# Kernel tuning notes

Hardware: AMD Instinct MI355X
Metric: run time of the kernel (lower is better)

Reference implementation:

```python
import jax, jax.numpy as jnp
import numpy as np

B, L = 16, 2048          # batch, raw history length
H, S, M = 512, 8, 512    # hidden_dim, sequence_count, max_seq_len
V = 32000                # shared embed_tokens vocab
TG = 64                  # TIME_GAP_BUCKET_COUNT
LN_EPS = 1e-5


def setup_inputs() -> dict:
    key = jax.random.key(0)
    ks = jax.random.split(key, 16)
    f = lambda k, shp, scale=0.02: jax.random.normal(k, shp, jnp.float32) * scale
    return {
        "history_tokens": jax.random.randint(ks[0], (B, L), 0, V),
        "history_post_tokens": jax.random.randint(ks[1], (B, L), 0, V),
        "history_author_tokens": jax.random.randint(ks[2], (B, L), 0, V),
        "history_action_tokens": jax.random.randint(ks[3], (B, L), 0, V),
        "history_time_gap": jax.random.randint(ks[4], (B, L), 0, TG + 1),
        "history_group_ids": jax.random.randint(ks[5], (B, L), 0, S + 1),
        "history_mask": jax.random.randint(ks[6], (B, L), 0, 2).astype(bool),
        "embed_table": f(ks[7], (V, H)),
        "time_gap_table": f(ks[8], (TG + 1, H)).at[0].set(0.0),   # padding_idx=0
        "seq_id_table": f(ks[9], (S + 1, H)).at[0].set(0.0),      # padding_idx=0
        "pos_table": f(ks[10], (M, H)),
        "ln_gamma": jnp.ones((5 * H,), jnp.float32),
        "ln_beta": jnp.zeros((5 * H,), jnp.float32),
        "w1": f(ks[11], (5 * H, 4 * H)),
        "b1": jnp.zeros((4 * H,), jnp.float32),
        "w2": f(ks[12], (4 * H, H)),
        "b2": jnp.zeros((H,), jnp.float32),
        "empty_tokens": f(ks[13], (S, H)),
    }


def _forward(embed_table, time_gap_table, seq_id_table, pos_table, ln_gamma, ln_beta,
             w1, b1, w2, b2, empty_tokens,
             history_tokens, history_post_tokens, history_author_tokens,
             history_action_tokens, history_time_gap, history_group_ids, history_mask):
    # --- event feature construction: 4 shared-vocab lookups + time-gap embedding ---
    h = embed_table[history_tokens]            # [B,L,H]
    p = embed_table[history_post_tokens]
    a = embed_table[history_author_tokens]
    act = embed_table[history_action_tokens]
    gap_idx = jnp.clip(history_time_gap, 0, TG)
    gap = time_gap_table[gap_idx] * (gap_idx != 0)[..., None]  # padding_idx=0 -> zero vec
    x = jnp.concatenate([h, p, a, act, gap], axis=-1)           # [B,L,5H]

    # --- event_projection: LayerNorm -> Linear -> SiLU -> (Dropout eval) -> Linear ---
    mu = x.mean(-1, keepdims=True)
    var = x.var(-1, keepdims=True)
    xn = (x - mu) * jax.lax.rsqrt(var + LN_EPS) * ln_gamma + ln_beta
    mid = jax.nn.silu(xn @ w1 + b1)                             # [B,L,4H]
    event = mid @ w2 + b2                                       # [B,L,H]

    # --- ragged regroup: for each (b, s) gather masked positions with group id s+1,
    #     keep the LAST M of them, scatter to slots 0..count-1 ---
    gid = history_group_ids                                     # [B,L]
    match = history_mask[:, None, :] & (gid[:, None, :] == jnp.arange(1, S + 1)[None, :, None])  # [B,S,L]
    cum = jnp.cumsum(match.astype(jnp.int32), axis=-1)          # rank+1 within group
    count = cum[..., -1]                                        # [B,S]
    offset = jnp.maximum(count - M, 0)                          # drop all but last M
    slot = cum - 1 - offset[..., None]                          # [B,S,L]
    keep = match & (slot >= 0)
    slot = jnp.where(keep, slot, M)                             # M is out-of-range -> dropped

    b_idx = jnp.arange(B)[:, None, None]
    s_idx = jnp.arange(S)[None, :, None]
    states = jnp.zeros((B, S, M, H), event.dtype)
    states = states.at[b_idx, s_idx, slot].set(event[:, None, :, :], mode="drop")
    smask = jnp.zeros((B, S, M), bool)
    smask = smask.at[b_idx, s_idx, slot].set(True, mode="drop")

    # empty groups get the learned empty token at slot 0
    empty = count == 0                                          # [B,S]
    states = states.at[:, :, 0, :].set(
        jnp.where(empty[..., None], empty_tokens[None], states[:, :, 0, :]))
    smask = smask.at[:, :, 0].set(smask[:, :, 0] | empty)

    # positional + sequence-id embeddings, then zero padded slots
    pos = pos_table[None, None]                                 # [1,1,M,H]
    sid = seq_id_table[1:S + 1][None, :, None, :]               # [1,S,1,H]
    states = (states + pos + sid) * smask[..., None].astype(states.dtype)
    return states, smask


def reference(history_tokens, history_post_tokens, history_author_tokens,
              history_action_tokens, history_time_gap, history_group_ids, history_mask,
              embed_table, time_gap_table, seq_id_table, pos_table, ln_gamma, ln_beta,
              w1, b1, w2, b2, empty_tokens):
    return _forward(embed_table, time_gap_table, seq_id_table, pos_table, ln_gamma, ln_beta,
                    w1, b1, w2, b2, empty_tokens,
                    history_tokens, history_post_tokens, history_author_tokens,
                    history_action_tokens, history_time_gap, history_group_ids, history_mask)
```

## Files before the change

kernel.cpp:

```cpp
#include <hip/hip_runtime.h>
#include <hip/hip_bf16.h>
#include <stdint.h>

#define B_ 16
#define L_ 2048
#define H_ 512
#define S_ 8
#define M_ 512
#define TG_ 64
#define NTOK (B_ * L_)
#define FIVEH (5 * H_)
#define FOURH (4 * H_)

typedef __attribute__((ext_vector_type(4))) float f32x4;
typedef __attribute__((ext_vector_type(8))) short bf16x8;

__device__ __forceinline__ short f2bf(float f) {
  unsigned u = __builtin_bit_cast(unsigned, f);
  unsigned r = (u + 0x7FFFu + ((u >> 16) & 1u)) >> 16;
  return (short)r;
}

__device__ __forceinline__ void gload_lds16(const void* g, void* l) {
  __builtin_amdgcn_global_load_lds(
      (const __attribute__((address_space(1))) unsigned int*)g,
      (__attribute__((address_space(3))) unsigned int*)l, 16, 0, 0);
}

#define BAR __builtin_amdgcn_s_barrier()
#define LGKM0 do { asm volatile("s_waitcnt lgkmcnt(0)" ::: "memory"); \
                   __builtin_amdgcn_sched_barrier(0); } while (0)
#define VMW(n) asm volatile("s_waitcnt vmcnt(" #n ")" ::: "memory")
#define PRIO(p) __builtin_amdgcn_s_setprio(p)


#define STAGE(src, isB, slot, half, kt) do {                                  \
    const short* _s = (src) + (size_t)((half) * 128) * K + (kt);              \
    const int _o = ((isB) ? 65536 : 0) + (slot) * 32768 + (half) * 16384;     \
    gload_lds16(_s + (size_t)sr0 * K + sc0, lds + _o + db0);                  \
    gload_lds16(_s + (size_t)sr1 * K + sc1, lds + _o + db1);                  \
  } while (0)

#define LDA(qr, slot) do { const int _b = (slot) * 32768 + aW + (qr) * 8192;  \
    _Pragma("unroll") for (int fm = 0; fm < 4; ++fm)                          \
    _Pragma("unroll") for (int ks = 0; ks < 2; ++ks)                          \
      a[fm][ks] = *(const bf16x8*)(lds + _b + sA[fm][ks]); } while (0)

#define LDB(dst, qc, slot) do { const int _b = (slot) * 32768 + bW + (qc) * 4096; \
    _Pragma("unroll") for (int fn = 0; fn < 2; ++fn)                          \
    _Pragma("unroll") for (int ks = 0; ks < 2; ++ks)                          \
      dst[fn][ks] = *(const bf16x8*)(lds + _b + sB[fn][ks]); } while (0)

#define MFMA16(qr, qc, bs) do {                                               \
    _Pragma("unroll") for (int fm = 0; fm < 4; ++fm)                          \
    _Pragma("unroll") for (int fn = 0; fn < 2; ++fn)                          \
    _Pragma("unroll") for (int ks = 0; ks < 2; ++ks)                          \
      acc[(qr)*4+fm][(qc)*2+fn] = __builtin_amdgcn_mfma_f32_16x16x32_bf16(    \
          a[fm][ks], bs[fn][ks], acc[(qr)*4+fm][(qc)*2+fn], 0, 0, 0); } while (0)

template<int K>
__device__ __forceinline__ void gemm_core(const short* __restrict__ Ag,
                                          const short* __restrict__ Bg,
                                          char* lds, f32x4 (&acc)[8][4],
                                          int tid) {
  constexpr int NITER = K / 128;
  const int lane = tid & 63;
  const int wave = tid >> 6;
  const int wm = wave >> 2;
  const int wn = wave & 3;
  const int la = lane & 15;
  const int hi = lane >> 4;

  const int x = (la & 7) << 4;
  int sA[4][2], sB[2][2];
#pragma unroll
  for (int fm = 0; fm < 4; ++fm)
#pragma unroll
    for (int ks = 0; ks < 2; ++ks)
      sA[fm][ks] = (((fm * 16 + la) * 128) + (ks * 32 + hi * 8) * 2) ^ x;
#pragma unroll
  for (int fn = 0; fn < 2; ++fn)
#pragma unroll
    for (int ks = 0; ks < 2; ++ks)
      sB[fn][ks] = ((((wn & 1) * 64 + fn * 16 + la) * 128) + (ks * 32 + hi * 8) * 2) ^ x;
  const int aW = wm * 16384;
  const int bW = 65536 + (wn >> 1) * 16384;

  const int db0 = tid * 16, db1 = tid * 16 + 8192;
  const int lb0 = db0 ^ (((db0 >> 7) & 7) << 4);
  const int lb1 = db1 ^ (((db1 >> 7) & 7) << 4);
  const int sr0 = lb0 >> 7, sc0 = (lb0 & 127) >> 1;
  const int sr1 = lb1 >> 7, sc1 = (lb1 & 127) >> 1;

  bf16x8 a[4][2], b0v[2][2], b1v[2][2];

  STAGE(Bg, 1, 0, 0, 0); STAGE(Bg, 1, 0, 1, 0);
  STAGE(Ag, 0, 0, 0, 0); STAGE(Ag, 0, 0, 1, 0);
  STAGE(Bg, 1, 1, 0, 64); STAGE(Bg, 1, 1, 1, 64);
  VMW(0);
  BAR;

  for (int i = 0; i < NITER - 1; ++i) {
    const int kt1 = (2 * i + 1) * 64, kt2 = kt1 + 64, kt3 = kt1 + 128;
    LDA(0, 0); LDB(b0v, 0, 0); STAGE(Ag, 0, 1, 0, kt1);
    BAR; LGKM0; PRIO(1); MFMA16(0, 0, b0v); PRIO(0); BAR;
    LDB(b1v, 1, 0); STAGE(Ag, 0, 1, 1, kt1);
    BAR; LGKM0; PRIO(1); MFMA16(0, 1, b1v); PRIO(0); BAR;
    LDA(1, 0); STAGE(Bg, 1, 0, 0, kt2);
    BAR; LGKM0; PRIO(1); MFMA16(1, 1, b1v); PRIO(0); BAR;
    STAGE(Bg, 1, 0, 1, kt2);
    BAR; LGKM0; PRIO(1); MFMA16(1, 0, b0v); PRIO(0); VMW(4); BAR;
    LDA(0, 1); LDB(b0v, 0, 1); STAGE(Ag, 0, 0, 0, kt2);
    BAR; LGKM0; PRIO(1); MFMA16(0, 0, b0v); PRIO(0); BAR;
    LDB(b1v, 1, 1); STAGE(Ag, 0, 0, 1, kt2);
    BAR; LGKM0; PRIO(1); MFMA16(0, 1, b1v); PRIO(0); BAR;
    LDA(1, 1); STAGE(Bg, 1, 1, 0, kt3);
    BAR; LGKM0; PRIO(1); MFMA16(1, 1, b1v); PRIO(0); BAR;
    STAGE(Bg, 1, 1, 1, kt3);
    BAR; LGKM0; PRIO(1); MFMA16(1, 0, b0v); PRIO(0); VMW(4); BAR;
  }
  {
    const int kt1 = (2 * (NITER - 1) + 1) * 64;
    LDA(0, 0); LDB(b0v, 0, 0); STAGE(Ag, 0, 1, 0, kt1);
    BAR; LGKM0; PRIO(1); MFMA16(0, 0, b0v); PRIO(0); BAR;
    LDB(b1v, 1, 0); STAGE(Ag, 0, 1, 1, kt1);
    BAR; LGKM0; PRIO(1); MFMA16(0, 1, b1v); PRIO(0); BAR;
    LDA(1, 0);
    BAR; LGKM0; PRIO(1); MFMA16(1, 1, b1v); PRIO(0); BAR;
    BAR; LGKM0; PRIO(1); MFMA16(1, 0, b0v); PRIO(0); VMW(0); BAR;
    LDA(0, 1); LDB(b0v, 0, 1);
    BAR; LGKM0; PRIO(1); MFMA16(0, 0, b0v); PRIO(0); BAR;
    LDB(b1v, 1, 1);
    BAR; LGKM0; PRIO(1); MFMA16(0, 1, b1v); PRIO(0); BAR;
    LDA(1, 1);
    BAR; LGKM0; PRIO(1); MFMA16(1, 1, b1v); PRIO(0); BAR;
    BAR; LGKM0; PRIO(1); MFMA16(1, 0, b0v); PRIO(0);
  }
}

__global__ __launch_bounds__(512, 2) void gemm1_kernel(
    const short* __restrict__ A, const short* __restrict__ Bt,
    const float* __restrict__ bias, const int* __restrict__ nkeep,
    short* __restrict__ C) {
  const int nbm = (nkeep[0] + 255) >> 8;
  const int local = blockIdx.x >> 3;
  if (local >= nbm) return;
  const int T = (blockIdx.x & 7) * nbm + local;
  const int bm = T >> 3, bn = T & 7;
  __shared__ __align__(16) char lds[131072];
  const int tid = threadIdx.x;
  f32x4 acc[8][4] = {};
  gemm_core<FIVEH>(A + (size_t)bm * 256 * FIVEH, Bt + (size_t)bn * 256 * FIVEH,
                   lds, acc, tid);
  const int lane = tid & 63, wave = tid >> 6;
  const int wm = wave >> 2, wn = wave & 3;
  const int la = lane & 15, hi = lane >> 4;
  const int row0 = bm * 256 + wm * 128 + hi * 4;
  const int col0 = bn * 256 + wn * 64 + la;
#pragma unroll
  for (int mi = 0; mi < 8; ++mi)
#pragma unroll
    for (int ni = 0; ni < 4; ++ni) {
      const int col = col0 + ni * 16;
      const float bv = bias[col];
#pragma unroll
      for (int r = 0; r < 4; ++r) {
        const int row = row0 + mi * 16 + r;
        float v = acc[mi][ni][r] + bv;
        float sg = 1.f / (1.f + __expf(-v));
        C[(size_t)row * FOURH + col] = f2bf(v * sg);
      }
    }
}

#define ASL(s) ((s) * 32768)
#define BSL(s) (98304 + (s) * 16384)

#define STG2(src, ldsoff, kt) do {                                            \
    const short* _s = (src) + (kt);                                          \
    gload_lds16(_s + (size_t)sr0 * 2048 + sc0, lds + (ldsoff) + db0);         \
    gload_lds16(_s + (size_t)sr1 * 2048 + sc1, lds + (ldsoff) + db1);         \
  } while (0)

#define LDA2(slot) do { const int _b = ASL(slot) + aW2;                       \
    _Pragma("unroll") for (int fm = 0; fm < 4; ++fm)                          \
    _Pragma("unroll") for (int ks = 0; ks < 2; ++ks)                          \
      a[fm][ks] = *(const bf16x8*)(lds + _b + sA2[fm][ks]); } while (0)

#define LDB2a(slot) do { const int _b = BSL(slot);                            \
    _Pragma("unroll") for (int fn = 0; fn < 2; ++fn)                          \
    _Pragma("unroll") for (int ks = 0; ks < 2; ++ks)                          \
      b[fn][ks] = *(const bf16x8*)(lds + _b + sB2[fn][ks]); } while (0)

#define LDB2b(slot) do { const int _b = BSL(slot);                            \
    _Pragma("unroll") for (int fn = 2; fn < 4; ++fn)                          \
    _Pragma("unroll") for (int ks = 0; ks < 2; ++ks)                          \
      b[fn][ks] = *(const bf16x8*)(lds + _b + sB2[fn][ks]); } while (0)

#define MFMA2(h) do {                                                         \
    _Pragma("unroll") for (int fm = 0; fm < 4; ++fm)                          \
    _Pragma("unroll") for (int fn = 2*(h); fn < 2*(h)+2; ++fn)                \
    _Pragma("unroll") for (int ks = 0; ks < 2; ++ks)                          \
      acc[fm][fn] = __builtin_amdgcn_mfma_f32_16x16x32_bf16(                  \
          a[fm][ks], b[fn][ks], acc[fm][fn], 0, 0, 0); } while (0)

#define T2(slot, kt, ISSUE, WAITC) do {                                       \
    LDA2(slot); LDB2a(slot);                                                  \
    if (ISSUE) STG2(Ag, ASL(((slot) + 2) % 3), kt);                           \
    BAR; LGKM0; PRIO(1); MFMA2(0); PRIO(0); BAR;                              \
    LDB2b(slot);                                                              \
    if (ISSUE) { STG2(Ag + 128 * 2048, ASL(((slot) + 2) % 3) + 16384, kt);    \
                 STG2(Bg, BSL(((slot) + 2) % 3), kt); }                       \
    BAR; LGKM0; PRIO(1); MFMA2(1); PRIO(0); WAITC; BAR;                       \
  } while (0)

__global__ __launch_bounds__(512) void gemm2fin_kernel(
    const short* __restrict__ A, const short* __restrict__ Bt,
    const float* __restrict__ b2, const float* __restrict__ pos,
    const float* __restrict__ sidtab, const int* __restrict__ destv,
    const int* __restrict__ nkeep, const int* __restrict__ counts,
    const float* __restrict__ empty_tok, float* __restrict__ states,
    float* __restrict__ smask) {
  if (blockIdx.x >= 512) {
    const int total = B_ * S_ * M_ * (H_ / 4);
    for (int idx = (blockIdx.x - 512) * 512 + threadIdx.x; idx < total;
         idx += 512 * 512) {
      const int row = idx >> 7, c = idx & 127;
      const int gs = row >> 9, m = row & (M_ - 1), s = gs & (S_ - 1);
      const int cnt = counts[gs];
      const bool empty = (cnt == 0);
      const bool filled = m < (cnt < M_ ? cnt : M_);
      if (c == 0) smask[row] = (filled || (empty && m == 0)) ? 1.0f : 0.0f;
      if (filled) continue;
      float4 o = make_float4(0.f, 0.f, 0.f, 0.f);
      if (empty && m == 0) {
        float4 e = ((const float4*)(empty_tok + s * H_))[c];
        float4 pv = ((const float4*)pos)[c];
        float4 sd = ((const float4*)(sidtab + (s + 1) * H_))[c];
        o.x = e.x + pv.x + sd.x;
        o.y = e.y + pv.y + sd.y;
        o.z = e.z + pv.z + sd.z;
        o.w = e.w + pv.w + sd.w;
      }
      ((float4*)(states + (size_t)row * H_))[c] = o;
    }
    return;
  }
  const int nk = nkeep[0];
  const int ntile = ((nk + 255) >> 8) << 2;
  const int q = ntile >> 3, r = ntile & 7;
  const int xg = blockIdx.x & 7, idx = blockIdx.x >> 3;
  const int cntx = q + (xg < r ? 1 : 0);
  if (idx >= cntx) return;
  const int T = xg * q + (xg < r ? xg : r) + idx;
  const int bm = T >> 2, bn = T & 3;
  __shared__ __align__(16) char lds[147456];
  const int tid = threadIdx.x;
  const int lane = tid & 63, wave = tid >> 6;
  const int wm = wave >> 1;
  const int wn = wave & 1;
  const int la = lane & 15, hi = lane >> 4;
  const short* Ag = A + (size_t)bm * 256 * 2048;
  const short* Bg = Bt + (size_t)bn * 128 * 2048;

  const int x = (la & 7) << 4;
  int sA2[4][2], sB2[4][2];
#pragma unroll
  for (int fm = 0; fm < 4; ++fm)
#pragma unroll
    for (int ks = 0; ks < 2; ++ks)
      sA2[fm][ks] = ((((wm & 1) * 64 + fm * 16 + la) * 128) + (ks * 32 + hi * 8) * 2) ^ x;
#pragma unroll
  for (int fn = 0; fn < 4; ++fn)
#pragma unroll
    for (int ks = 0; ks < 2; ++ks)
      sB2[fn][ks] = (((wn * 64 + fn * 16 + la) * 128) + (ks * 32 + hi * 8) * 2) ^ x;
  const int aW2 = (wm >> 1) * 16384;

  const int db0 = tid * 16, db1 = tid * 16 + 8192;
  const int lb0 = db0 ^ (((db0 >> 7) & 7) << 4);
  const int lb1 = db1 ^ (((db1 >> 7) & 7) << 4);
  const int sr0 = lb0 >> 7, sc0 = (lb0 & 127) >> 1;
  const int sr1 = lb1 >> 7, sc1 = (lb1 & 127) >> 1;

  f32x4 acc[4][4] = {};
  bf16x8 a[4][2], b[4][2];

  STG2(Ag, ASL(0), 0); STG2(Ag + 128 * 2048, ASL(0) + 16384, 0); STG2(Bg, BSL(0), 0);
  STG2(Ag, ASL(1), 64); STG2(Ag + 128 * 2048, ASL(1) + 16384, 64); STG2(Bg, BSL(1), 64);
  VMW(6);
  BAR;
  for (int i = 0; i < 10; ++i) {
    const int kt = i * 192 + 128;
    T2(0, kt, true, VMW(6));
    T2(1, kt + 64, true, VMW(6));
    T2(2, kt + 128, true, VMW(6));
  }
  T2(0, 0, false, VMW(0));
  T2(1, 0, false, ((void)0));

  const int row0 = bm * 256 + wm * 64 + hi * 4;
  const int col0 = bn * 128 + wn * 64 + la;
#pragma unroll
  for (int mi = 0; mi < 4; ++mi) {
#pragma unroll
    for (int r2 = 0; r2 < 4; ++r2) {
      const int row = row0 + mi * 16 + r2;
      if (row >= nk) continue;
      const int dest = destv[row];
      const int slot = dest & (M_ - 1);
      const int gs = dest >> 9;
      const int s = gs & (S_ - 1);
      float* orow = states + (size_t)dest * H_;
#pragma unroll
      for (int n = 0; n < 4; ++n) {
        const int col = col0 + n * 16;
        orow[col] = acc[mi][n][r2] + b2[col] + pos[slot * H_ + col] +
                    sidtab[(s + 1) * H_ + col];
      }
    }
  }
}

__global__ __launch_bounds__(256) void prep_kernel(
    const float* __restrict__ w1, short* __restrict__ w1T,
    const float* __restrict__ w2, short* __restrict__ w2T,
    const int* __restrict__ gid, const int* __restrict__ mask,
    int* __restrict__ counts, int* __restrict__ tokidx,
    int* __restrict__ destv, int* __restrict__ nkeep) {
  const int bid = blockIdx.x;
  if (bid < 6144) {
    const float* in;
    short* out;
    int K, N, tt;
    if (bid < 5120) { in = w1; out = w1T; K = FIVEH; N = FOURH; tt = bid; }
    else            { in = w2; out = w2T; K = FOURH; N = H_;   tt = bid - 5120; }
    const int nT = N >> 5;
    const int n0 = (tt % nT) * 32, k0 = (tt / nT) * 32;
    __shared__ float tile[32][33];
    const int tx = threadIdx.x & 31, ty = threadIdx.x >> 5;
#pragma unroll
    for (int i = 0; i < 32; i += 8)
      tile[ty + i][tx] = in[(size_t)(k0 + ty + i) * N + n0 + tx];
    __syncthreads();
#pragma unroll
    for (int i = 0; i < 32; i += 8)
      out[(size_t)(n0 + ty + i) * K + k0 + tx] = f2bf(tile[tx][ty + i]);
    return;
  }
  const int grp = bid - 6144;
  const int b = grp >> 3;
  const int s = grp & 7;
  const int g = s + 1;
  const int base = b * L_;
  const int t = threadIdx.x;
  int loc = 0, sum = 0;
  const int l0 = t * 8;
#pragma unroll
  for (int j = 0; j < 8; ++j) {
    int l = l0 + j;
    bool mt = (mask[base + l] != 0) && (gid[base + l] == g);
    loc |= (mt ? 1 : 0) << j;
    sum += mt ? 1 : 0;
  }
  __shared__ int sdata[256];
  __shared__ int basep, offs;
  sdata[t] = sum;
  __syncthreads();
  for (int off = 1; off < 256; off <<= 1) {
    int vv = (t >= off) ? sdata[t - off] : 0;
    __syncthreads();
    sdata[t] += vv;
    __syncthreads();
  }
  if (t == 255) {
    const int cnt = sdata[255];
    counts[grp] = cnt;
    const int kc = cnt < M_ ? cnt : M_;
    offs = cnt - kc;
    basep = atomicAdd(nkeep, kc);
  }
  __syncthreads();
  int run = sdata[t] - sum;
  const int gsM = grp * M_;
#pragma unroll
  for (int j = 0; j < 8; ++j) {
    if ((loc >> j) & 1) {
      run += 1;
      const int slot = run - 1 - offs;
      if (slot >= 0) {
        tokidx[basep + slot] = base + l0 + j;
        destv[basep + slot] = gsM + slot;
      }
    }
  }
}

__global__ __launch_bounds__(256) void gather_ln_kernel(
    const int* __restrict__ tokidx, const int* __restrict__ nkeep,
    const int* __restrict__ tok0, const int* __restrict__ tok1,
    const int* __restrict__ tok2, const int* __restrict__ tok3,
    const int* __restrict__ tgap,
    const float* __restrict__ emb, const float* __restrict__ gaptab,
    const float* __restrict__ gamma, const float* __restrict__ beta,
    short* __restrict__ xn) {
  const int wid = threadIdx.x >> 6;
  const int l = threadIdx.x & 63;
  const int j = blockIdx.x * 4 + wid;
  const int nk = nkeep[0];
  const int padded = (nk + 255) & ~255;
  if (j >= padded) return;
  short* orow = xn + (size_t)j * FIVEH;
  if (j >= nk) {
    short4 z = make_short4(0, 0, 0, 0);
#pragma unroll
    for (int i = 0; i < 10; ++i) ((short4*)orow)[i * 64 + l] = z;
    return;
  }
  const int token = tokidx[j];
  const int tk0 = tok0[token], tk1 = tok1[token], tk2 = tok2[token],
            tk3 = tok3[token];
  int gi = tgap[token];
  gi = gi < 0 ? 0 : (gi > TG_ ? TG_ : gi);
  const float4* sb[5];
  sb[0] = (const float4*)(emb + (size_t)tk0 * H_);
  sb[1] = (const float4*)(emb + (size_t)tk1 * H_);
  sb[2] = (const float4*)(emb + (size_t)tk2 * H_);
  sb[3] = (const float4*)(emb + (size_t)tk3 * H_);
  sb[4] = (const float4*)(gaptab + (size_t)gi * H_);
  float4 v[10];
  float sum = 0.f, sq = 0.f;
#pragma unroll
  for (int i = 0; i < 10; ++i) {
    const int d4 = i * 64 + l;
    const int seg = i >> 1;
    float4 xv;
    if (seg < 4 || gi != 0) xv = sb[seg][d4 & 127];
    else xv = make_float4(0.f, 0.f, 0.f, 0.f);
    v[i] = xv;
    sum += xv.x + xv.y + xv.z + xv.w;
    sq += xv.x * xv.x + xv.y * xv.y + xv.z * xv.z + xv.w * xv.w;
  }
#pragma unroll
  for (int s = 32; s; s >>= 1) {
    sum += __shfl_xor(sum, s, 64);
    sq += __shfl_xor(sq, s, 64);
  }
  const float mu = sum * (1.f / FIVEH);
  const float var = sq * (1.f / FIVEH) - mu * mu;
  const float rs = rsqrtf(var + 1e-5f);
#pragma unroll
  for (int i = 0; i < 10; ++i) {
    const int d4 = i * 64 + l;
    const float4 g4 = ((const float4*)gamma)[d4];
    const float4 b4 = ((const float4*)beta)[d4];
    short4 o;
    o.x = f2bf((v[i].x - mu) * rs * g4.x + b4.x);
    o.y = f2bf((v[i].y - mu) * rs * g4.y + b4.y);
    o.z = f2bf((v[i].z - mu) * rs * g4.z + b4.z);
    o.w = f2bf((v[i].w - mu) * rs * g4.w + b4.w);
    ((short4*)orow)[d4] = o;
  }
}

extern "C" void kernel_launch(void* const* d_in, const int* in_sizes, int n_in,
                              void* d_out, int out_size, void* d_ws, size_t ws_size,
                              hipStream_t stream) {
  const int* tok0 = (const int*)d_in[0];
  const int* tok1 = (const int*)d_in[1];
  const int* tok2 = (const int*)d_in[2];
  const int* tok3 = (const int*)d_in[3];
  const int* tgap = (const int*)d_in[4];
  const int* gid = (const int*)d_in[5];
  const int* mask = (const int*)d_in[6];
  const float* emb = (const float*)d_in[7];
  const float* gaptab = (const float*)d_in[8];
  const float* sidtab = (const float*)d_in[9];
  const float* pos = (const float*)d_in[10];
  const float* gamma = (const float*)d_in[11];
  const float* beta = (const float*)d_in[12];
  const float* w1 = (const float*)d_in[13];
  const float* b1 = (const float*)d_in[14];
  const float* w2 = (const float*)d_in[15];
  const float* b2 = (const float*)d_in[16];
  const float* empty_tok = (const float*)d_in[17];

  char* p = (char*)d_ws;
  short* xn = (short*)p;  p += (size_t)NTOK * FIVEH * 2;
  short* mid = (short*)p; p += (size_t)NTOK * FOURH * 2;
  short* w1T = (short*)p; p += (size_t)FOURH * FIVEH * 2;
  short* w2T = (short*)p; p += (size_t)H_ * FOURH * 2;
  int* tokidx = (int*)p;  p += (size_t)NTOK * 4;
  int* destv = (int*)p;   p += (size_t)NTOK * 4;
  int* counts = (int*)p;  p += 512;
  int* nkeep = (int*)p;   p += 512;

  float* states = (float*)d_out;
  float* smask = states + (size_t)B_ * S_ * M_ * H_;

  hipMemsetAsync(nkeep, 0, 4, stream);
  prep_kernel<<<6272, 256, 0, stream>>>(w1, w1T, w2, w2T, gid, mask, counts,
                                        tokidx, destv, nkeep);
  gather_ln_kernel<<<NTOK / 4, 256, 0, stream>>>(tokidx, nkeep, tok0, tok1, tok2,
                                                 tok3, tgap, emb, gaptab, gamma,
                                                 beta, xn);
  gemm1_kernel<<<128 * 8, 512, 0, stream>>>(xn, w1T, b1, nkeep, mid);
  gemm2fin_kernel<<<512 + 512, 512, 0, stream>>>(mid, w2T, b2, pos, sidtab,
                                                 destv, nkeep, counts, empty_tok,
                                                 states, smask);
}
```

Measured before the change: 259.9 us.

## Rebalance kernel stages: move weight transpose into gather, fill into gemm1

Splits the scan out of the prep kernel into a small standalone kernel and moves the weight fp32-to-bf16 transposes into the gather/LayerNorm launch, so they run alongside the gather work. The padding/empty-slot fill of states and smask moves from the gemm2 launch into the gemm1 launch, using the idle blocks beyond the active tile count plus 64 extra blocks. The goal is to put the memory-bound side work onto otherwise idle CUs during the GEMM and gather phases and shorten the critical path. The trade-off is an extra kernel launch and possible contention with the GEMM blocks for bandwidth.

```diff
diff --git a/kernel.cpp b/kernel.cpp
--- a/kernel.cpp
+++ b/kernel.cpp
@@ -138,93 +138,22 @@
   }
 }
 
-__global__ __launch_bounds__(512, 2) void gemm1_kernel(
+__global__ __launch_bounds__(512, 2) void gemm1fin_kernel(
     const short* __restrict__ A, const short* __restrict__ Bt,
     const float* __restrict__ bias, const int* __restrict__ nkeep,
-    short* __restrict__ C) {
+    short* __restrict__ C, const int* __restrict__ counts,
+    const float* __restrict__ empty_tok, const float* __restrict__ pos,
+    const float* __restrict__ sidtab, float* __restrict__ states,
+    float* __restrict__ smask) {
   const int nbm = (nkeep[0] + 255) >> 8;
   const int local = blockIdx.x >> 3;
-  if (local >= nbm) return;
-  const int T = (blockIdx.x & 7) * nbm + local;
-  const int bm = T >> 3, bn = T & 7;
-  __shared__ __align__(16) char lds[131072];
-  const int tid = threadIdx.x;
-  f32x4 acc[8][4] = {};
-  gemm_core<FIVEH>(A + (size_t)bm * 256 * FIVEH, Bt + (size_t)bn * 256 * FIVEH,
-                   lds, acc, tid);
-  const int lane = tid & 63, wave = tid >> 6;
-  const int wm = wave >> 2, wn = wave & 3;
-  const int la = lane & 15, hi = lane >> 4;
-  const int row0 = bm * 256 + wm * 128 + hi * 4;
-  const int col0 = bn * 256 + wn * 64 + la;
-#pragma unroll
-  for (int mi = 0; mi < 8; ++mi)
-#pragma unroll
-    for (int ni = 0; ni < 4; ++ni) {
-      const int col = col0 + ni * 16;
-      const float bv = bias[col];
-#pragma unroll
-      for (int r = 0; r < 4; ++r) {
-        const int row = row0 + mi * 16 + r;
-        float v = acc[mi][ni][r] + bv;
-        float sg = 1.f / (1.f + __expf(-v));
-        C[(size_t)row * FOURH + col] = f2bf(v * sg);
-      }
-    }
-}
-
-#define ASL(s) ((s) * 32768)
-#define BSL(s) (98304 + (s) * 16384)
-
-#define STG2(src, ldsoff, kt) do {                                            \
-    const short* _s = (src) + (kt);                                          \
-    gload_lds16(_s + (size_t)sr0 * 2048 + sc0, lds + (ldsoff) + db0);         \
-    gload_lds16(_s + (size_t)sr1 * 2048 + sc1, lds + (ldsoff) + db1);         \
-  } while (0)
-
-#define LDA2(slot) do { const int _b = ASL(slot) + aW2;                       \
-    _Pragma("unroll") for (int fm = 0; fm < 4; ++fm)                          \
-    _Pragma("unroll") for (int ks = 0; ks < 2; ++ks)                          \
-      a[fm][ks] = *(const bf16x8*)(lds + _b + sA2[fm][ks]); } while (0)
-
-#define LDB2a(slot) do { const int _b = BSL(slot);                            \
-    _Pragma("unroll") for (int fn = 0; fn < 2; ++fn)                          \
-    _Pragma("unroll") for (int ks = 0; ks < 2; ++ks)                          \
-      b[fn][ks] = *(const bf16x8*)(lds + _b + sB2[fn][ks]); } while (0)
-
-#define LDB2b(slot) do { const int _b = BSL(slot);                            \
-    _Pragma("unroll") for (int fn = 2; fn < 4; ++fn)                          \
-    _Pragma("unroll") for (int ks = 0; ks < 2; ++ks)                          \
-      b[fn][ks] = *(const bf16x8*)(lds + _b + sB2[fn][ks]); } while (0)
-
-#define MFMA2(h) do {                                                         \
-    _Pragma("unroll") for (int fm = 0; fm < 4; ++fm)                          \
-    _Pragma("unroll") for (int fn = 2*(h); fn < 2*(h)+2; ++fn)                \
-    _Pragma("unroll") for (int ks = 0; ks < 2; ++ks)                          \
-      acc[fm][fn] = __builtin_amdgcn_mfma_f32_16x16x32_bf16(                  \
-          a[fm][ks], b[fn][ks], acc[fm][fn], 0, 0, 0); } while (0)
-
-#define T2(slot, kt, ISSUE, WAITC) do {                                       \
-    LDA2(slot); LDB2a(slot);                                                  \
-    if (ISSUE) STG2(Ag, ASL(((slot) + 2) % 3), kt);                           \
-    BAR; LGKM0; PRIO(1); MFMA2(0); PRIO(0); BAR;                              \
-    LDB2b(slot);                                                              \
-    if (ISSUE) { STG2(Ag + 128 * 2048, ASL(((slot) + 2) % 3) + 16384, kt);    \
-                 STG2(Bg, BSL(((slot) + 2) % 3), kt); }                       \
-    BAR; LGKM0; PRIO(1); MFMA2(1); PRIO(0); WAITC; BAR;                       \
-  } while (0)
-
-__global__ __launch_bounds__(512) void gemm2fin_kernel(
-    const short* __restrict__ A, const short* __restrict__ Bt,
-    const float* __restrict__ b2, const float* __restrict__ pos,
-    const float* __restrict__ sidtab, const int* __restrict__ destv,
-    const int* __restrict__ nkeep, const int* __restrict__ counts,
-    const float* __restrict__ empty_tok, float* __restrict__ states,
-    float* __restrict__ smask) {
-  if (blockIdx.x >= 512) {
+  if (local >= nbm) {
+    const int fstart = nbm << 3;
+    const int fcount = (int)gridDim.x - fstart;
+    const int fid = (int)blockIdx.x - fstart;
     const int total = B_ * S_ * M_ * (H_ / 4);
-    for (int idx = (blockIdx.x - 512) * 512 + threadIdx.x; idx < total;
-         idx += 512 * 512) {
+    for (int idx = fid * 512 + (int)threadIdx.x; idx < total;
+         idx += fcount * 512) {
       const int row = idx >> 7, c = idx & 127;
       const int gs = row >> 9, m = row & (M_ - 1), s = gs & (S_ - 1);
       const int cnt = counts[gs];
@@ -246,6 +175,80 @@
     }
     return;
   }
+  const int T = (blockIdx.x & 7) * nbm + local;
+  const int bm = T >> 3, bn = T & 7;
+  __shared__ __align__(16) char lds[131072];
+  const int tid = threadIdx.x;
+  f32x4 acc[8][4] = {};
+  gemm_core<FIVEH>(A + (size_t)bm * 256 * FIVEH, Bt + (size_t)bn * 256 * FIVEH,
+                   lds, acc, tid);
+  const int lane = tid & 63, wave = tid >> 6;
+  const int wm = wave >> 2, wn = wave & 3;
+  const int la = lane & 15, hi = lane >> 4;
+  const int row0 = bm * 256 + wm * 128 + hi * 4;
+  const int col0 = bn * 256 + wn * 64 + la;
+#pragma unroll
+  for (int mi = 0; mi < 8; ++mi)
+#pragma unroll
+    for (int ni = 0; ni < 4; ++ni) {
+      const int col = col0 + ni * 16;
+      const float bv = bias[col];
+#pragma unroll
+      for (int r = 0; r < 4; ++r) {
+        const int row = row0 + mi * 16 + r;
+        float v = acc[mi][ni][r] + bv;
+        float sg = 1.f / (1.f + __expf(-v));
+        C[(size_t)row * FOURH + col] = f2bf(v * sg);
+      }
+    }
+}
+
+#define ASL(s) ((s) * 32768)
+#define BSL(s) (98304 + (s) * 16384)
+
+#define STG2(src, ldsoff, kt) do {                                            \
+    const short* _s = (src) + (kt);                                          \
+    gload_lds16(_s + (size_t)sr0 * 2048 + sc0, lds + (ldsoff) + db0);         \
+    gload_lds16(_s + (size_t)sr1 * 2048 + sc1, lds + (ldsoff) + db1);         \
+  } while (0)
+
+#define LDA2(slot) do { const int _b = ASL(slot) + aW2;                       \
+    _Pragma("unroll") for (int fm = 0; fm < 4; ++fm)                          \
+    _Pragma("unroll") for (int ks = 0; ks < 2; ++ks)                          \
+      a[fm][ks] = *(const bf16x8*)(lds + _b + sA2[fm][ks]); } while (0)
+
+#define LDB2a(slot) do { const int _b = BSL(slot);                            \
+    _Pragma("unroll") for (int fn = 0; fn < 2; ++fn)                          \
+    _Pragma("unroll") for (int ks = 0; ks < 2; ++ks)                          \
+      b[fn][ks] = *(const bf16x8*)(lds + _b + sB2[fn][ks]); } while (0)
+
+#define LDB2b(slot) do { const int _b = BSL(slot);                            \
+    _Pragma("unroll") for (int fn = 2; fn < 4; ++fn)                          \
+    _Pragma("unroll") for (int ks = 0; ks < 2; ++ks)                          \
+      b[fn][ks] = *(const bf16x8*)(lds + _b + sB2[fn][ks]); } while (0)
+
+#define MFMA2(h) do {                                                         \
+    _Pragma("unroll") for (int fm = 0; fm < 4; ++fm)                          \
+    _Pragma("unroll") for (int fn = 2*(h); fn < 2*(h)+2; ++fn)                \
+    _Pragma("unroll") for (int ks = 0; ks < 2; ++ks)                          \
+      acc[fm][fn] = __builtin_amdgcn_mfma_f32_16x16x32_bf16(                  \
+          a[fm][ks], b[fn][ks], acc[fm][fn], 0, 0, 0); } while (0)
+
+#define T2(slot, kt, ISSUE, WAITC) do {                                       \
+    LDA2(slot); LDB2a(slot);                                                  \
+    if (ISSUE) STG2(Ag, ASL(((slot) + 2) % 3), kt);                           \
+    BAR; LGKM0; PRIO(1); MFMA2(0); PRIO(0); BAR;                              \
+    LDB2b(slot);                                                              \
+    if (ISSUE) { STG2(Ag + 128 * 2048, ASL(((slot) + 2) % 3) + 16384, kt);    \
+                 STG2(Bg, BSL(((slot) + 2) % 3), kt); }                       \
+    BAR; LGKM0; PRIO(1); MFMA2(1); PRIO(0); WAITC; BAR;                       \
+  } while (0)
+
+__global__ __launch_bounds__(512) void gemm2_kernel(
+    const short* __restrict__ A, const short* __restrict__ Bt,
+    const float* __restrict__ b2, const float* __restrict__ pos,
+    const float* __restrict__ sidtab, const int* __restrict__ destv,
+    const int* __restrict__ nkeep, float* __restrict__ states) {
   const int nk = nkeep[0];
   const int ntile = ((nk + 255) >> 8) << 2;
   const int q = ntile >> 3, r = ntile & 7;
@@ -322,14 +325,70 @@
   }
 }
 
-__global__ __launch_bounds__(256) void prep_kernel(
-    const float* __restrict__ w1, short* __restrict__ w1T,
-    const float* __restrict__ w2, short* __restrict__ w2T,
+__global__ __launch_bounds__(256) void scan_kernel(
     const int* __restrict__ gid, const int* __restrict__ mask,
     int* __restrict__ counts, int* __restrict__ tokidx,
     int* __restrict__ destv, int* __restrict__ nkeep) {
-  const int bid = blockIdx.x;
-  if (bid < 6144) {
+  const int grp = blockIdx.x;
+  const int b = grp >> 3;
+  const int s = grp & 7;
+  const int g = s + 1;
+  const int base = b * L_;
+  const int t = threadIdx.x;
+  int loc = 0, sum = 0;
+  const int l0 = t * 8;
+#pragma unroll
+  for (int j = 0; j < 8; ++j) {
+    int l = l0 + j;
+    bool mt = (mask[base + l] != 0) && (gid[base + l] == g);
+    loc |= (mt ? 1 : 0) << j;
+    sum += mt ? 1 : 0;
+  }
+  __shared__ int sdata[256];
+  __shared__ int basep, offs;
+  sdata[t] = sum;
+  __syncthreads();
+  for (int off = 1; off < 256; off <<= 1) {
+    int vv = (t >= off) ? sdata[t - off] : 0;
+    __syncthreads();
+    sdata[t] += vv;
+    __syncthreads();
+  }
+  if (t == 255) {
+    const int cnt = sdata[255];
+    counts[grp] = cnt;
+    const int kc = cnt < M_ ? cnt : M_;
+    offs = cnt - kc;
+    basep = atomicAdd(nkeep, kc);
+  }
+  __syncthreads();
+  int run = sdata[t] - sum;
+  const int gsM = grp * M_;
+#pragma unroll
+  for (int j = 0; j < 8; ++j) {
+    if ((loc >> j) & 1) {
+      run += 1;
+      const int slot = run - 1 - offs;
+      if (slot >= 0) {
+        tokidx[basep + slot] = base + l0 + j;
+        destv[basep + slot] = gsM + slot;
+      }
+    }
+  }
+}
+
+__global__ __launch_bounds__(256) void gather_tr_kernel(
+    const int* __restrict__ tokidx, const int* __restrict__ nkeep,
+    const int* __restrict__ tok0, const int* __restrict__ tok1,
+    const int* __restrict__ tok2, const int* __restrict__ tok3,
+    const int* __restrict__ tgap,
+    const float* __restrict__ emb, const float* __restrict__ gaptab,
+    const float* __restrict__ gamma, const float* __restrict__ beta,
+    short* __restrict__ xn,
+    const float* __restrict__ w1, short* __restrict__ w1T,
+    const float* __restrict__ w2, short* __restrict__ w2T) {
+  if (blockIdx.x >= 8192) {
+    const int bid = blockIdx.x - 8192;
     const float* in;
     short* out;
     int K, N, tt;
@@ -348,62 +407,6 @@
       out[(size_t)(n0 + ty + i) * K + k0 + tx] = f2bf(tile[tx][ty + i]);
     return;
   }
-  const int grp = bid - 6144;
-  const int b = grp >> 3;
-  const int s = grp & 7;
-  const int g = s + 1;
-  const int base = b * L_;
-  const int t = threadIdx.x;
-  int loc = 0, sum = 0;
-  const int l0 = t * 8;
-#pragma unroll
-  for (int j = 0; j < 8; ++j) {
-    int l = l0 + j;
-    bool mt = (mask[base + l] != 0) && (gid[base + l] == g);
-    loc |= (mt ? 1 : 0) << j;
-    sum += mt ? 1 : 0;
-  }
-  __shared__ int sdata[256];
-  __shared__ int basep, offs;
-  sdata[t] = sum;
-  __syncthreads();
-  for (int off = 1; off < 256; off <<= 1) {
-    int vv = (t >= off) ? sdata[t - off] : 0;
-    __syncthreads();
-    sdata[t] += vv;
-    __syncthreads();
-  }
-  if (t == 255) {
-    const int cnt = sdata[255];
-    counts[grp] = cnt;
-    const int kc = cnt < M_ ? cnt : M_;
-    offs = cnt - kc;
-    basep = atomicAdd(nkeep, kc);
-  }
-  __syncthreads();
-  int run = sdata[t] - sum;
-  const int gsM = grp * M_;
-#pragma unroll
-  for (int j = 0; j < 8; ++j) {
-    if ((loc >> j) & 1) {
-      run += 1;
-      const int slot = run - 1 - offs;
-      if (slot >= 0) {
-        tokidx[basep + slot] = base + l0 + j;
-        destv[basep + slot] = gsM + slot;
-      }
-    }
-  }
-}
-
-__global__ __launch_bounds__(256) void gather_ln_kernel(
-    const int* __restrict__ tokidx, const int* __restrict__ nkeep,
-    const int* __restrict__ tok0, const int* __restrict__ tok1,
-    const int* __restrict__ tok2, const int* __restrict__ tok3,
-    const int* __restrict__ tgap,
-    const float* __restrict__ emb, const float* __restrict__ gaptab,
-    const float* __restrict__ gamma, const float* __restrict__ beta,
-    short* __restrict__ xn) {
   const int wid = threadIdx.x >> 6;
   const int l = threadIdx.x & 63;
   const int j = blockIdx.x * 4 + wid;
@@ -499,13 +502,14 @@
   float* smask = states + (size_t)B_ * S_ * M_ * H_;
 
   hipMemsetAsync(nkeep, 0, 4, stream);
-  prep_kernel<<<6272, 256, 0, stream>>>(w1, w1T, w2, w2T, gid, mask, counts,
-                                        tokidx, destv, nkeep);
-  gather_ln_kernel<<<NTOK / 4, 256, 0, stream>>>(tokidx, nkeep, tok0, tok1, tok2,
-                                                 tok3, tgap, emb, gaptab, gamma,
-                                                 beta, xn);
-  gemm1_kernel<<<128 * 8, 512, 0, stream>>>(xn, w1T, b1, nkeep, mid);
-  gemm2fin_kernel<<<512 + 512, 512, 0, stream>>>(mid, w2T, b2, pos, sidtab,
-                                                 destv, nkeep, counts, empty_tok,
+  scan_kernel<<<B_ * S_, 256, 0, stream>>>(gid, mask, counts, tokidx, destv,
+                                           nkeep);
+  gather_tr_kernel<<<8192 + 6144, 256, 0, stream>>>(
+      tokidx, nkeep, tok0, tok1, tok2, tok3, tgap, emb, gaptab, gamma, beta,
+      xn, w1, w1T, w2, w2T);
+  gemm1fin_kernel<<<1024 + 64, 512, 0, stream>>>(xn, w1T, b1, nkeep, mid,
+                                                 counts, empty_tok, pos, sidtab,
                                                  states, smask);
-}
+  gemm2_kernel<<<512, 512, 0, stream>>>(mid, w2T, b2, pos, sidtab, destv,
+                                        nkeep, states);
+}
```

Result: faster. 252.5 us (-2.8%).
